# Optimization experiments

Hardware: AMD Instinct MI355X
Metric: run time of the kernel (lower is better)

## Reference

```python
import jax, jax.numpy as jnp
import numpy as np

N_NODES = 100000
IN_CH = 64
HID = 128
N_EDGES = 1600000


def sage_conv(x, src, dst, Wl, bl, Wr, num_nodes):
    # PyG SAGEConv (mean aggr): out = lin_l(mean_{j->i} x_j) + lin_r(x_i)
    msg = x[src]                                           # [E, F] gather
    agg = jax.ops.segment_sum(msg, dst, num_segments=num_nodes)   # [N, F]
    cnt = jax.ops.segment_sum(jnp.ones((src.shape[0],), x.dtype), dst,
                              num_segments=num_nodes)      # [N]
    mean = agg / jnp.maximum(cnt, 1.0)[:, None]
    return mean @ Wl.T + bl + x @ Wr.T


def setup_inputs() -> dict:
    key = jax.random.key(0)
    k1, k2, k3, k4, k5, k6, k7, k8 = jax.random.split(key, 8)
    x = jax.random.normal(k1, (N_NODES, IN_CH), dtype=jnp.float32)
    edge_index = jax.random.randint(k2, (2, N_EDGES), 0, N_NODES, dtype=jnp.int64)
    s1 = 1.0 / np.sqrt(IN_CH)
    s2 = 1.0 / np.sqrt(HID)
    Wl1 = jax.random.uniform(k3, (HID, IN_CH), jnp.float32, -s1, s1)
    bl1 = jax.random.uniform(k4, (HID,), jnp.float32, -s1, s1)
    Wr1 = jax.random.uniform(k5, (HID, IN_CH), jnp.float32, -s1, s1)
    Wl2 = jax.random.uniform(k6, (HID, HID), jnp.float32, -s2, s2)
    bl2 = jax.random.uniform(k7, (HID,), jnp.float32, -s2, s2)
    Wr2 = jax.random.uniform(k8, (HID, HID), jnp.float32, -s2, s2)
    return {"x": x, "edge_index": edge_index,
            "Wl1": Wl1, "bl1": bl1, "Wr1": Wr1,
            "Wl2": Wl2, "bl2": bl2, "Wr2": Wr2}


def reference(x, edge_index, Wl1, bl1, Wr1, Wl2, bl2, Wr2):
    src, dst = edge_index[0], edge_index[1]
    n = x.shape[0]
    h = sage_conv(x, src, dst, Wl1, bl1, Wr1, n)
    h = jax.nn.relu(h)
    # dropout p=0.2 is identity in eval/reference mode
    out = sage_conv(h, src, dst, Wl2, bl2, Wr2, n)
    return out
```

## Files before the change

kernel.cpp:

```cpp
#include <hip/hip_runtime.h>
#include <hip/hip_bf16.h>
#include <stdint.h>

#define NN 100000
#define EE 1600000
#define NBUCK 196
#define CSB 512

typedef __attribute__((ext_vector_type(4))) float f32x4;
typedef __attribute__((ext_vector_type(8))) short bf16x8;

__device__ inline ushort f2bf(float f) {
    union { float f; uint32_t u; } v; v.f = f;
    uint32_t u = v.u;
    uint32_t r = (u + 0x7fffu + ((u >> 16) & 1u)) >> 16;
    return (ushort)r;
}
__device__ inline float bflo(uint32_t u) {
    union { uint32_t u; float f; } v; v.u = u << 16; return v.f;
}
__device__ inline float bfhi(uint32_t u) {
    union { uint32_t u; float f; } v; v.u = u & 0xffff0000u; return v.f;
}

__global__ void detect_kernel(const unsigned int* raw, int* flag) {
    int i = blockIdx.x * blockDim.x + threadIdx.x;
    if (i < 4096) {
        if (raw[2 * i + 1] != 0u) atomicOr(flag, 1);
    }
}

__global__ void cvt_f32_bf16(const float* __restrict__ in, ushort* __restrict__ out, int n4) {
    int i = blockIdx.x * blockDim.x + threadIdx.x;
    if (i >= n4) return;
    float4 v = *(const float4*)&in[i * 4];
    ushort o[4] = { f2bf(v.x), f2bf(v.y), f2bf(v.z), f2bf(v.w) };
    *(uint64_t*)&out[i * 4] = *(const uint64_t*)o;
}

__global__ void build_wcat(const float* __restrict__ Wl, const float* __restrict__ Wr,
                           ushort* __restrict__ Wcat, int K) {
    int t = blockIdx.x * blockDim.x + threadIdx.x;
    int KT = 2 * K;
    if (t >= 128 * KT) return;
    int o = t / KT, k = t % KT;
    float v = (k < K) ? Wl[o * K + k] : Wr[o * K + (k - K)];
    Wcat[o * KT + k] = f2bf(v);
}

__global__ __launch_bounds__(256) void coarse_hist(const void* raw, const int* flag,
                                                   int* ccnt, int E) {
    __shared__ int lh[NBUCK];
    for (int i = threadIdx.x; i < NBUCK; i += 256) lh[i] = 0;
    __syncthreads();
    int stride = gridDim.x * 256;
    if (*flag) {
        const int* p = (const int*)raw;
        for (int e = blockIdx.x * 256 + threadIdx.x; e < E; e += stride)
            atomicAdd(&lh[p[E + e] >> 9], 1);
    } else {
        const long long* p = (const long long*)raw;
        for (int e = blockIdx.x * 256 + threadIdx.x; e < E; e += stride)
            atomicAdd(&lh[((int)p[E + e]) >> 9], 1);
    }
    __syncthreads();
    for (int i = threadIdx.x; i < NBUCK; i += 256)
        if (lh[i]) atomicAdd(&ccnt[i], lh[i]);
}

__global__ void coarse_scan(const int* ccnt, int* coff, int* offsets, int E) {
    __shared__ int part[256];
    int t = threadIdx.x;
    int v[4]; int s = 0;
    #pragma unroll
    for (int j = 0; j < 4; j++) {
        int i = t * 4 + j;
        v[j] = (i < NBUCK) ? ccnt[i] : 0;
        s += v[j];
    }
    part[t] = s; __syncthreads();
    for (int off = 1; off < 256; off <<= 1) {
        int add = (t >= off) ? part[t - off] : 0;
        __syncthreads();
        part[t] += add;
        __syncthreads();
    }
    int run = part[t] - s;
    #pragma unroll
    for (int j = 0; j < 4; j++) {
        int i = t * 4 + j;
        if (i <= NBUCK) coff[i] = run;
        run += v[j];
    }
    if (t == 0) offsets[NN] = E;
}

__global__ __launch_bounds__(256) void coarse_scatter2(const void* raw, const int* flag,
                                                       const int* coff, int* cfill,
                                                       uint32_t* pbuf, int E) {
    __shared__ int lh[NBUCK];
    __shared__ int gbase[NBUCK];
    __shared__ int lfill[NBUCK];
    const int t = threadIdx.x;
    for (int i = t; i < NBUCK; i += 256) { lh[i] = 0; lfill[i] = 0; }
    __syncthreads();
    const int chunk = (E + (int)gridDim.x - 1) / (int)gridDim.x;
    const int s0 = blockIdx.x * chunk;
    const int s1 = min(E, s0 + chunk);
    const bool is32 = (*flag != 0);
    if (is32) {
        const int* p = (const int*)raw;
        for (int e = s0 + t; e < s1; e += 256) atomicAdd(&lh[p[E + e] >> 9], 1);
    } else {
        const long long* p = (const long long*)raw;
        for (int e = s0 + t; e < s1; e += 256) atomicAdd(&lh[((int)p[E + e]) >> 9], 1);
    }
    __syncthreads();
    for (int i = t; i < NBUCK; i += 256)
        gbase[i] = coff[i] + (lh[i] ? atomicAdd(&cfill[i], lh[i]) : 0);
    __syncthreads();
    if (is32) {
        const int* p = (const int*)raw;
        for (int e = s0 + t; e < s1; e += 256) {
            int sr = p[e], d = p[E + e];
            int b = d >> 9;
            int r = atomicAdd(&lfill[b], 1);
            pbuf[gbase[b] + r] = ((uint32_t)(d & 511) << 17) | (uint32_t)sr;
        }
    } else {
        const long long* p = (const long long*)raw;
        for (int e = s0 + t; e < s1; e += 256) {
            int sr = (int)p[e], d = (int)p[E + e];
            int b = d >> 9;
            int r = atomicAdd(&lfill[b], 1);
            pbuf[gbase[b] + r] = ((uint32_t)(d & 511) << 17) | (uint32_t)sr;
        }
    }
}

__global__ __launch_bounds__(512) void fine_bucket(const uint32_t* __restrict__ pbuf,
                                                   const int* __restrict__ coff,
                                                   int* __restrict__ offsets,
                                                   int* __restrict__ srcs_sort, int N) {
    __shared__ int cnt[512], sc[512], fil[512];
    const int b = blockIdx.x, t = threadIdx.x;
    const int s = coff[b], e = coff[b + 1];
    cnt[t] = 0; fil[t] = 0;
    __syncthreads();
    for (int i = s + t; i < e; i += 512) atomicAdd(&cnt[pbuf[i] >> 17], 1);
    __syncthreads();
    sc[t] = cnt[t];
    __syncthreads();
    for (int off = 1; off < 512; off <<= 1) {
        int add = (t >= off) ? sc[t - off] : 0;
        __syncthreads();
        sc[t] += add;
        __syncthreads();
    }
    const int nb0 = b * 512;
    if (nb0 + t < N) offsets[nb0 + t] = s + sc[t] - cnt[t];
    for (int i = s + t; i < e; i += 512) {
        uint32_t p = pbuf[i];
        int dl = (int)(p >> 17);
        int sr = (int)(p & 0x1FFFFu);
        int pos = s + (sc[dl] - cnt[dl]) + atomicAdd(&fil[dl], 1);
        srcs_sort[pos] = sr;
    }
}

template<int K, bool RELU, bool OUT_BF16>
__global__ __launch_bounds__(256) void sage_fused(
    const int* __restrict__ offsets, const int* __restrict__ srcs,
    const ushort* __restrict__ xin, const ushort* __restrict__ Wcat,
    const float* __restrict__ bl, void* __restrict__ outv, int N)
{
    constexpr int KT = 2 * K;
    constexpr int RP = K + 8;
    __shared__ ushort mlds[32][RP];
    __shared__ ushort slds[32][RP];
    const int t = threadIdx.x;
    const int w = t >> 6;
    const int lane = t & 63;
    const int nb = blockIdx.x * 32;

    #pragma unroll
    for (int idx = t; idx < 32 * (K / 8); idx += 256) {
        int r = idx / (K / 8), c = idx % (K / 8);
        *(uint4*)&slds[r][c * 8] = *(const uint4*)&xin[(size_t)(nb + r) * K + c * 8];
    }

    const int half = lane >> 5;
    const int sl = lane & 31;

    for (int i = 0; i < 8; i++) {
        const int ln = w * 8 + i;
        const int node = nb + ln;
        int s0 = offsets[node], s1 = offsets[node + 1];
        float inv = 1.0f / fmaxf((float)(s1 - s0), 1.0f);

        if (K == 64) {
            float ax0=0.f, ay0=0.f, ax1=0.f, ay1=0.f, ax2=0.f, ay2=0.f, ax3=0.f, ay3=0.f;
            for (int base = s0; base < s1; base += 64) {
                int cnt = min(64, s1 - base);
                int myidx = (base + lane < s1) ? srcs[base + lane] : 0;
                int j = 0;
                for (; j + 8 <= cnt; j += 8) {
                    int sA = __shfl(myidx, j + half);
                    int sB = __shfl(myidx, j + 2 + half);
                    int sC = __shfl(myidx, j + 4 + half);
                    int sD = __shfl(myidx, j + 6 + half);
                    uint32_t uA = *(const uint32_t*)&xin[(size_t)sA * 64 + sl * 2];
                    uint32_t uB = *(const uint32_t*)&xin[(size_t)sB * 64 + sl * 2];
                    uint32_t uC = *(const uint32_t*)&xin[(size_t)sC * 64 + sl * 2];
                    uint32_t uD = *(const uint32_t*)&xin[(size_t)sD * 64 + sl * 2];
                    ax0 += bflo(uA); ay0 += bfhi(uA);
                    ax1 += bflo(uB); ay1 += bfhi(uB);
                    ax2 += bflo(uC); ay2 += bfhi(uC);
                    ax3 += bflo(uD); ay3 += bfhi(uD);
                }
                for (; j + 2 <= cnt; j += 2) {
                    int s = __shfl(myidx, j + half);
                    uint32_t u = *(const uint32_t*)&xin[(size_t)s * 64 + sl * 2];
                    ax0 += bflo(u); ay0 += bfhi(u);
                }
                int st = __shfl(myidx, j & 63);
                if (j < cnt && half == 0) {
                    uint32_t u = *(const uint32_t*)&xin[(size_t)st * 64 + sl * 2];
                    ax0 += bflo(u); ay0 += bfhi(u);
                }
            }
            float ax = ax0 + ax1 + ax2 + ax3;
            float ay = ay0 + ay1 + ay2 + ay3;
            ax += __shfl_xor(ax, 32);
            ay += __shfl_xor(ay, 32);
            if (half == 0) {
                ushort o[2] = { f2bf(ax * inv), f2bf(ay * inv) };
                *(uint32_t*)&mlds[ln][sl * 2] = *(const uint32_t*)o;
            }
        } else {
            float a0=0.f, a1=0.f, a2=0.f, a3=0.f;
            float b0=0.f, b1=0.f, b2=0.f, b3=0.f;
            float c0=0.f, c1=0.f, c2=0.f, c3=0.f;
            float d0=0.f, d1=0.f, d2=0.f, d3=0.f;
            for (int base = s0; base < s1; base += 64) {
                int cnt = min(64, s1 - base);
                int myidx = (base + lane < s1) ? srcs[base + lane] : 0;
                int j = 0;
                for (; j + 8 <= cnt; j += 8) {
                    int sA = __shfl(myidx, j + half);
                    int sB = __shfl(myidx, j + 2 + half);
                    int sC = __shfl(myidx, j + 4 + half);
                    int sD = __shfl(myidx, j + 6 + half);
                    uint2 uA = *(const uint2*)&xin[(size_t)sA * 128 + sl * 4];
                    uint2 uB = *(const uint2*)&xin[(size_t)sB * 128 + sl * 4];
                    uint2 uC = *(const uint2*)&xin[(size_t)sC * 128 + sl * 4];
                    uint2 uD = *(const uint2*)&xin[(size_t)sD * 128 + sl * 4];
                    a0 += bflo(uA.x); a1 += bfhi(uA.x); a2 += bflo(uA.y); a3 += bfhi(uA.y);
                    b0 += bflo(uB.x); b1 += bfhi(uB.x); b2 += bflo(uB.y); b3 += bfhi(uB.y);
                    c0 += bflo(uC.x); c1 += bfhi(uC.x); c2 += bflo(uC.y); c3 += bfhi(uC.y);
                    d0 += bflo(uD.x); d1 += bfhi(uD.x); d2 += bflo(uD.y); d3 += bfhi(uD.y);
                }
                for (; j + 2 <= cnt; j += 2) {
                    int s = __shfl(myidx, j + half);
                    uint2 u = *(const uint2*)&xin[(size_t)s * 128 + sl * 4];
                    a0 += bflo(u.x); a1 += bfhi(u.x); a2 += bflo(u.y); a3 += bfhi(u.y);
                }
                int st = __shfl(myidx, j & 63);
                if (j < cnt && half == 0) {
                    uint2 u = *(const uint2*)&xin[(size_t)st * 128 + sl * 4];
                    a0 += bflo(u.x); a1 += bfhi(u.x); a2 += bflo(u.y); a3 += bfhi(u.y);
                }
            }
            float v0 = a0 + b0 + c0 + d0;
            float v1 = a1 + b1 + c1 + d1;
            float v2 = a2 + b2 + c2 + d2;
            float v3 = a3 + b3 + c3 + d3;
            v0 += __shfl_xor(v0, 32);
            v1 += __shfl_xor(v1, 32);
            v2 += __shfl_xor(v2, 32);
            v3 += __shfl_xor(v3, 32);
            if (half == 0) {
                ushort o[4] = { f2bf(v0 * inv), f2bf(v1 * inv), f2bf(v2 * inv), f2bf(v3 * inv) };
                *(uint64_t*)&mlds[ln][sl * 4] = *(const uint64_t*)o;
            }
        }
    }
    __syncthreads();

    const int lrow = lane & 15;
    const int lgrp = lane >> 4;
    f32x4 acc[2][2];
    #pragma unroll
    for (int nt = 0; nt < 2; nt++)
        #pragma unroll
        for (int ct = 0; ct < 2; ct++)
            acc[nt][ct] = (f32x4){0.f, 0.f, 0.f, 0.f};

    #pragma unroll
    for (int ks = 0; ks < KT; ks += 32) {
        const int ac = (ks < K) ? ks : (ks - K);
        const ushort* Xb = (ks < K) ? &mlds[0][0] : &slds[0][0];
        bf16x8 x0 = *(const bf16x8*)&Xb[(lrow) * RP + ac + lgrp * 8];
        bf16x8 x1 = *(const bf16x8*)&Xb[(16 + lrow) * RP + ac + lgrp * 8];
        bf16x8 wA = *(const bf16x8*)&Wcat[(size_t)(w * 32 + lrow) * KT + ks + lgrp * 8];
        bf16x8 wB = *(const bf16x8*)&Wcat[(size_t)(w * 32 + 16 + lrow) * KT + ks + lgrp * 8];
        acc[0][0] = __builtin_amdgcn_mfma_f32_16x16x32_bf16(wA, x0, acc[0][0], 0, 0, 0);
        acc[0][1] = __builtin_amdgcn_mfma_f32_16x16x32_bf16(wB, x0, acc[0][1], 0, 0, 0);
        acc[1][0] = __builtin_amdgcn_mfma_f32_16x16x32_bf16(wA, x1, acc[1][0], 0, 0, 0);
        acc[1][1] = __builtin_amdgcn_mfma_f32_16x16x32_bf16(wB, x1, acc[1][1], 0, 0, 0);
    }

    #pragma unroll
    for (int ct = 0; ct < 2; ct++) {
        const int ch0 = w * 32 + ct * 16 + lgrp * 4;
        float4 b4 = *(const float4*)&bl[ch0];
        #pragma unroll
        for (int nt = 0; nt < 2; nt++) {
            int n = nb + nt * 16 + lrow;
            float v0 = acc[nt][ct][0] + b4.x;
            float v1 = acc[nt][ct][1] + b4.y;
            float v2 = acc[nt][ct][2] + b4.z;
            float v3 = acc[nt][ct][3] + b4.w;
            if (RELU) {
                v0 = fmaxf(v0, 0.f); v1 = fmaxf(v1, 0.f);
                v2 = fmaxf(v2, 0.f); v3 = fmaxf(v3, 0.f);
            }
            if (OUT_BF16) {
                ushort o[4] = { f2bf(v0), f2bf(v1), f2bf(v2), f2bf(v3) };
                *(uint64_t*)&((ushort*)outv)[(size_t)n * 128 + ch0] = *(const uint64_t*)o;
            } else {
                float4 o = make_float4(v0, v1, v2, v3);
                *(float4*)&((float*)outv)[(size_t)n * 128 + ch0] = o;
            }
        }
    }
}

extern "C" void kernel_launch(void* const* d_in, const int* in_sizes, int n_in,
                              void* d_out, int out_size, void* d_ws, size_t ws_size,
                              hipStream_t stream) {
    const float* x   = (const float*)d_in[0];
    const void*  er  = d_in[1];
    const float* Wl1 = (const float*)d_in[2];
    const float* bl1 = (const float*)d_in[3];
    const float* Wr1 = (const float*)d_in[4];
    const float* Wl2 = (const float*)d_in[5];
    const float* bl2 = (const float*)d_in[6];
    const float* Wr2 = (const float*)d_in[7];
    float* out = (float*)d_out;

    const int N = NN, E = EE;

    char* ws = (char*)d_ws;
    size_t off = 0;
    auto carve = [&](size_t bytes) { char* p = ws + off; off += (bytes + 511) & ~(size_t)511; return p; };
    int*      flag      = (int*)     carve(4);
    int*      ccnt      = (int*)     carve((size_t)NBUCK * 4);
    int*      cfill     = (int*)     carve((size_t)NBUCK * 4);
    int*      coff      = (int*)     carve((size_t)(NBUCK + 1) * 4);
    uint32_t* pbuf      = (uint32_t*)carve((size_t)E * 4);
    int*      offsets   = (int*)     carve((size_t)(N + 1) * 4);
    int*      srcs_sort = (int*)     carve((size_t)E * 4);
    ushort*   xb        = (ushort*)  carve((size_t)N * 64 * 2);
    ushort*   hb        = (ushort*)  carve((size_t)N * 128 * 2);
    ushort*   wc1       = (ushort*)  carve((size_t)128 * 128 * 2);
    ushort*   wc2       = (ushort*)  carve((size_t)128 * 256 * 2);
    (void)ws_size;

    hipMemsetAsync(flag, 0, 4, stream);
    hipMemsetAsync(ccnt, 0, (size_t)NBUCK * 4, stream);
    hipMemsetAsync(cfill, 0, (size_t)NBUCK * 4, stream);

    detect_kernel<<<16, 256, 0, stream>>>((const unsigned int*)er, flag);

    cvt_f32_bf16<<<(N * 64 / 4 + 255) / 256, 256, 0, stream>>>(x, xb, N * 64 / 4);
    build_wcat<<<(128 * 128 + 255) / 256, 256, 0, stream>>>(Wl1, Wr1, wc1, 64);
    build_wcat<<<(128 * 256 + 255) / 256, 256, 0, stream>>>(Wl2, Wr2, wc2, 128);

    coarse_hist<<<512, 256, 0, stream>>>(er, flag, ccnt, E);
    coarse_scan<<<1, 256, 0, stream>>>(ccnt, coff, offsets, E);
    coarse_scatter2<<<CSB, 256, 0, stream>>>(er, flag, coff, cfill, pbuf, E);
    fine_bucket<<<NBUCK, 512, 0, stream>>>(pbuf, coff, offsets, srcs_sort, N);

    const int fb = N / 32;

    sage_fused<64, true, true><<<fb, 256, 0, stream>>>(offsets, srcs_sort, xb, wc1, bl1, hb, N);
    sage_fused<128, false, false><<<fb, 256, 0, stream>>>(offsets, srcs_sort, hb, wc2, bl2, out, N);
}
```

Measured before the change: 218.7 us.

## Process two nodes per wavefront, one per half-wave, in neighbor aggregation

```diff
diff --git a/kernel.cpp b/kernel.cpp
--- a/kernel.cpp
+++ b/kernel.cpp
@@ -191,66 +191,61 @@
 
     const int half = lane >> 5;
     const int sl = lane & 31;
-
-    for (int i = 0; i < 8; i++) {
-        const int ln = w * 8 + i;
-        const int node = nb + ln;
-        int s0 = offsets[node], s1 = offsets[node + 1];
-        float inv = 1.0f / fmaxf((float)(s1 - s0), 1.0f);
+    const int hbase = lane & 32;
+
+    int offv = 0;
+    if (lane < 9) offv = offsets[nb + w * 8 + lane];
+
+    for (int pi = 0; pi < 4; pi++) {
+        const int ln = w * 8 + pi * 2 + half;
+        const int s0 = __shfl(offv, pi * 2 + half);
+        const int s1 = __shfl(offv, pi * 2 + half + 1);
+        const float inv = 1.0f / fmaxf((float)(s1 - s0), 1.0f);
 
         if (K == 64) {
-            float ax0=0.f, ay0=0.f, ax1=0.f, ay1=0.f, ax2=0.f, ay2=0.f, ax3=0.f, ay3=0.f;
-            for (int base = s0; base < s1; base += 64) {
-                int cnt = min(64, s1 - base);
-                int myidx = (base + lane < s1) ? srcs[base + lane] : 0;
+            float x0=0.f, y0=0.f, x1=0.f, y1=0.f, x2=0.f, y2=0.f, x3=0.f, y3=0.f;
+            for (int base = s0; base < s1; base += 32) {
+                int cnt = min(32, s1 - base);
+                int myidx = (base + sl < s1) ? srcs[base + sl] : 0;
                 int j = 0;
-                for (; j + 8 <= cnt; j += 8) {
-                    int sA = __shfl(myidx, j + half);
-                    int sB = __shfl(myidx, j + 2 + half);
-                    int sC = __shfl(myidx, j + 4 + half);
-                    int sD = __shfl(myidx, j + 6 + half);
+                for (; j + 4 <= cnt; j += 4) {
+                    int sA = __shfl(myidx, hbase + j);
+                    int sB = __shfl(myidx, hbase + j + 1);
+                    int sC = __shfl(myidx, hbase + j + 2);
+                    int sD = __shfl(myidx, hbase + j + 3);
                     uint32_t uA = *(const uint32_t*)&xin[(size_t)sA * 64 + sl * 2];
                     uint32_t uB = *(const uint32_t*)&xin[(size_t)sB * 64 + sl * 2];
                     uint32_t uC = *(const uint32_t*)&xin[(size_t)sC * 64 + sl * 2];
                     uint32_t uD = *(const uint32_t*)&xin[(size_t)sD * 64 + sl * 2];
-                    ax0 += bflo(uA); ay0 += bfhi(uA);
-                    ax1 += bflo(uB); ay1 += bfhi(uB);
-                    ax2 += bflo(uC); ay2 += bfhi(uC);
-                    ax3 += bflo(uD); ay3 += bfhi(uD);
+                    x0 += bflo(uA); y0 += bfhi(uA);
+                    x1 += bflo(uB); y1 += bfhi(uB);
+                    x2 += bflo(uC); y2 += bfhi(uC);
+                    x3 += bflo(uD); y3 += bfhi(uD);
                 }
-                for (; j + 2 <= cnt; j += 2) {
-                    int s = __shfl(myidx, j + half);
+                for (; j < cnt; j++) {
+                    int s = __shfl(myidx, hbase + j);
                     uint32_t u = *(const uint32_t*)&xin[(size_t)s * 64 + sl * 2];
-                    ax0 += bflo(u); ay0 += bfhi(u);
-                }
-                int st = __shfl(myidx, j & 63);
-                if (j < cnt && half == 0) {
-                    uint32_t u = *(const uint32_t*)&xin[(size_t)st * 64 + sl * 2];
-                    ax0 += bflo(u); ay0 += bfhi(u);
+                    x0 += bflo(u); y0 += bfhi(u);
                 }
             }
-            float ax = ax0 + ax1 + ax2 + ax3;
-            float ay = ay0 + ay1 + ay2 + ay3;
-            ax += __shfl_xor(ax, 32);
-            ay += __shfl_xor(ay, 32);
-            if (half == 0) {
-                ushort o[2] = { f2bf(ax * inv), f2bf(ay * inv) };
-                *(uint32_t*)&mlds[ln][sl * 2] = *(const uint32_t*)o;
-            }
+            float ax = x0 + x1 + x2 + x3;
+            float ay = y0 + y1 + y2 + y3;
+            ushort o[2] = { f2bf(ax * inv), f2bf(ay * inv) };
+            *(uint32_t*)&mlds[ln][sl * 2] = *(const uint32_t*)o;
         } else {
             float a0=0.f, a1=0.f, a2=0.f, a3=0.f;
             float b0=0.f, b1=0.f, b2=0.f, b3=0.f;
             float c0=0.f, c1=0.f, c2=0.f, c3=0.f;
             float d0=0.f, d1=0.f, d2=0.f, d3=0.f;
-            for (int base = s0; base < s1; base += 64) {
-                int cnt = min(64, s1 - base);
-                int myidx = (base + lane < s1) ? srcs[base + lane] : 0;
+            for (int base = s0; base < s1; base += 32) {
+                int cnt = min(32, s1 - base);
+                int myidx = (base + sl < s1) ? srcs[base + sl] : 0;
                 int j = 0;
-                for (; j + 8 <= cnt; j += 8) {
-                    int sA = __shfl(myidx, j + half);
-                    int sB = __shfl(myidx, j + 2 + half);
-                    int sC = __shfl(myidx, j + 4 + half);
-                    int sD = __shfl(myidx, j + 6 + half);
+                for (; j + 4 <= cnt; j += 4) {
+                    int sA = __shfl(myidx, hbase + j);
+                    int sB = __shfl(myidx, hbase + j + 1);
+                    int sC = __shfl(myidx, hbase + j + 2);
+                    int sD = __shfl(myidx, hbase + j + 3);
                     uint2 uA = *(const uint2*)&xin[(size_t)sA * 128 + sl * 4];
                     uint2 uB = *(const uint2*)&xin[(size_t)sB * 128 + sl * 4];
                     uint2 uC = *(const uint2*)&xin[(size_t)sC * 128 + sl * 4];
@@ -260,14 +255,9 @@
                     c0 += bflo(uC.x); c1 += bfhi(uC.x); c2 += bflo(uC.y); c3 += bfhi(uC.y);
                     d0 += bflo(uD.x); d1 += bfhi(uD.x); d2 += bflo(uD.y); d3 += bfhi(uD.y);
                 }
-                for (; j + 2 <= cnt; j += 2) {
-                    int s = __shfl(myidx, j + half);
+                for (; j < cnt; j++) {
+                    int s = __shfl(myidx, hbase + j);
                     uint2 u = *(const uint2*)&xin[(size_t)s * 128 + sl * 4];
-                    a0 += bflo(u.x); a1 += bfhi(u.x); a2 += bflo(u.y); a3 += bfhi(u.y);
-                }
-                int st = __shfl(myidx, j & 63);
-                if (j < cnt && half == 0) {
-                    uint2 u = *(const uint2*)&xin[(size_t)st * 128 + sl * 4];
                     a0 += bflo(u.x); a1 += bfhi(u.x); a2 += bflo(u.y); a3 += bfhi(u.y);
                 }
             }
@@ -275,14 +265,8 @@
             float v1 = a1 + b1 + c1 + d1;
             float v2 = a2 + b2 + c2 + d2;
             float v3 = a3 + b3 + c3 + d3;
-            v0 += __shfl_xor(v0, 32);
-            v1 += __shfl_xor(v1, 32);
-            v2 += __shfl_xor(v2, 32);
-            v3 += __shfl_xor(v3, 32);
-            if (half == 0) {
-                ushort o[4] = { f2bf(v0 * inv), f2bf(v1 * inv), f2bf(v2 * inv), f2bf(v3 * inv) };
-                *(uint64_t*)&mlds[ln][sl * 4] = *(const uint64_t*)o;
-            }
+            ushort o[4] = { f2bf(v0 * inv), f2bf(v1 * inv), f2bf(v2 * inv), f2bf(v3 * inv) };
+            *(uint64_t*)&mlds[ln][sl * 4] = *(const uint64_t*)o;
         }
     }
     __syncthreads();
```

Result: faster. 210.4 us (-3.8%).
